# Kernel tuning notes

Measured on AMD Instinct MI355X. Metric: run time of the kernel, lower is better.

## Reference

```python
import math
import jax, jax.numpy as jnp
from jax import lax
import numpy as np

D = 128            # head_dim
B = 16             # independent KV streams (e.g., heads)
S = 4096           # update sequence length
P = 4096           # reconstruction positions
MAX_SEQ_LEN = 8192
# (n_waves, ema_rate, freq_low, freq_high) per level, coarse -> fine
LEVELS = [(16, 0.001, 0.01, 1.0), (32, 0.005, 0.5, 3.0), (64, 0.02, 1.0, 6.0), (128, 0.05, 2.0, 10.0), (256, 0.1, 4.0, 20.0)]
TWO_PI = 2.0 * math.pi


def setup_inputs() -> dict:
    key = jax.random.key(0)
    ks = jax.random.split(key, 2 + len(LEVELS))
    inp = {}
    inp['kv_vectors'] = jax.random.normal(ks[0], (B, S, D), dtype=jnp.float32)
    inp['positions'] = jnp.arange(S, dtype=jnp.int32)
    inp['recon_positions'] = jnp.sort(jax.random.randint(ks[1], (P,), 0, MAX_SEQ_LEN, dtype=jnp.int32))
    for i, (n, a, lo, hi) in enumerate(LEVELS):
        k1, k2 = jax.random.split(ks[2 + i], 2)
        inp[f'W_enc_{i}'] = jax.random.normal(k1, (3 * n, D), dtype=jnp.float32) / math.sqrt(D)
        inp[f'W_dec_{i}'] = jax.random.normal(k2, (D, n), dtype=jnp.float32) / math.sqrt(n)
        inp[f'base_freqs_{i}'] = jnp.linspace(lo, hi, n, dtype=jnp.float32)
    return inp


def _ema_final(x, alpha):
    # x: [S, ...]; returns EMA state after S sequential steps from zero init.
    def step(c, xt):
        return (1.0 - alpha) * c + alpha * xt, None
    final, _ = lax.scan(step, jnp.zeros(x.shape[1:], x.dtype), x)
    return final


def _forward(kv_vectors, positions, recon_positions, params):
    pos_norm = positions.astype(jnp.float32)[:, None] / MAX_SEQ_LEN    # [S,1]
    rpos_norm = recon_positions.astype(jnp.float32)[:, None] / MAX_SEQ_LEN  # [P,1]
    out = jnp.zeros((kv_vectors.shape[0], recon_positions.shape[0], D), jnp.float32)
    for (n, alpha, _lo, _hi), (W_enc, W_dec, base_freqs) in zip(LEVELS, params):
        deltas = jnp.einsum('bsd,wd->bsw', kv_vectors, W_enc)          # [B,S,3n]
        d_freq, d_amp, d_phase = jnp.split(deltas, 3, axis=-1)         # each [B,S,n]
        pos_signal = jnp.sin(base_freqs[None, :] * pos_norm * TWO_PI)  # [S,n]
        xs = jnp.stack([d_freq * pos_signal[None], jnp.abs(d_amp), d_phase], axis=0)  # [3,B,S,n]
        xs = jnp.transpose(xs, (2, 0, 1, 3))                           # [S,3,B,n]
        freqs, amps, phases = _ema_final(xs, alpha)                    # each [B,n]
        wave_phases = TWO_PI * (freqs[:, None, :] + base_freqs[None, None, :]) * rpos_norm[None] + phases[:, None, :]
        wave_values = amps[:, None, :] * jnp.sin(wave_phases)          # [B,P,n]
        out = out + jnp.einsum('bpn,dn->bpd', wave_values, W_dec)
    return out


def reference(kv_vectors, positions, recon_positions,
              W_enc_0, W_dec_0, base_freqs_0,
              W_enc_1, W_dec_1, base_freqs_1,
              W_enc_2, W_dec_2, base_freqs_2,
              W_enc_3, W_dec_3, base_freqs_3,
              W_enc_4, W_dec_4, base_freqs_4):
    params = [(W_enc_0, W_dec_0, base_freqs_0), (W_enc_1, W_dec_1, base_freqs_1),
              (W_enc_2, W_dec_2, base_freqs_2), (W_enc_3, W_dec_3, base_freqs_3),
              (W_enc_4, W_dec_4, base_freqs_4)]
    return _forward(kv_vectors, positions, recon_positions, params)
```

## Files before the change

### kernel.cpp

```cpp
#include <hip/hip_runtime.h>

typedef __attribute__((ext_vector_type(8))) short short8;
typedef __attribute__((ext_vector_type(4))) float floatx4;

#define B_   16
#define S_   4096
#define D_   128
#define P_   4096
#define CTOT 496
#define BP   (B_ * CTOT)
#define WPADG 512
#define INV2PI 0.15915494309189535f
#define NWAVE_B 132
#define NJB 33

__device__ __forceinline__ unsigned short f2bf(float f) {
    unsigned u = __float_as_uint(f);
    u += 0x7fffu + ((u >> 16) & 1u);
    return (unsigned short)(u >> 16);
}
__device__ __forceinline__ unsigned int pack2(float a, float b) {
    return (unsigned int)f2bf(a) | ((unsigned int)f2bf(b) << 16);
}

__global__ __launch_bounds__(256) void encoder(
    const float* __restrict__ kv, const int* __restrict__ positions,
    const float* __restrict__ we0, const float* __restrict__ we1,
    const float* __restrict__ we2, const float* __restrict__ we3,
    const float* __restrict__ we4,
    const float* __restrict__ wd0, const float* __restrict__ wd1,
    const float* __restrict__ wd2, const float* __restrict__ wd3,
    const float* __restrict__ wd4,
    const float* __restrict__ bf0, const float* __restrict__ bf1,
    const float* __restrict__ bf2, const float* __restrict__ bf3,
    const float* __restrict__ bf4,
    float* __restrict__ accb,
    unsigned short* __restrict__ wdbT)
{
    const int tid = threadIdx.x;

    if (blockIdx.y == 0) {
        int g = blockIdx.x * 256 + tid;
        int k0 = g * 8;
        if (k0 < D_ * WPADG) {
            int d = k0 >> 9, w0g = k0 & 511;
            union { unsigned int u[4]; short8 s; } r;
            if (w0g >= CTOT) {
                r.u[0] = r.u[1] = r.u[2] = r.u[3] = 0;
            } else {
                const float* src; int off, nl;
                if (w0g < 16)       { src = wd0; off = 0;   nl = 16;  }
                else if (w0g < 48)  { src = wd1; off = 16;  nl = 32;  }
                else if (w0g < 112) { src = wd2; off = 48;  nl = 64;  }
                else if (w0g < 240) { src = wd3; off = 112; nl = 128; }
                else                { src = wd4; off = 240; nl = 256; }
                const float* p = src + (size_t)d * nl + (w0g - off);
                float4 a = *(const float4*)(p);
                float4 c = *(const float4*)(p + 4);
                r.u[0] = pack2(a.x, a.y); r.u[1] = pack2(a.z, a.w);
                r.u[2] = pack2(c.x, c.y); r.u[3] = pack2(c.z, c.w);
            }
            *(short8*)(wdbT + k0) = r.s;
        }
    }

    const int b    = blockIdx.y;
    const int rem  = blockIdx.x * 4 + (tid >> 6);
    const int lane = tid & 63, ln15 = lane & 15, quad = lane >> 4;

    int bx, widx, nw;
    if (rem < 40)      { bx = rem / 10;               widx = rem % 10; nw = 10; }
    else if (rem < 60) { int r = rem - 40; bx = 4 + r / 5; widx = r % 5; nw = 5; }
    else if (rem < 84) { int r = rem - 60; bx = 8 + r / 3; widx = r % 3; nw = 3; }
    else               { bx = 16 + (rem - 84);        widx = 0;        nw = 1; }
    const int t0  = S_ - 64 * (bx + 1);
    const int cnt = (bx < 4) ? 93 : (bx < 8) ? 45 : (bx < 16) ? 21 : 9;

    const float* arow = kv + ((size_t)(b * S_ + t0 + ln15)) * D_ + quad * 8;
    short8 afr[4][4];
    #pragma unroll
    for (int m = 0; m < 4; ++m)
        #pragma unroll
        for (int k = 0; k < 4; ++k) {
            float4 x = *(const float4*)(arow + m * 16 * D_ + k * 32);
            float4 y = *(const float4*)(arow + m * 16 * D_ + k * 32 + 4);
            union { unsigned int u[4]; short8 s; } r;
            r.u[0] = pack2(x.x, x.y); r.u[1] = pack2(x.z, x.w);
            r.u[2] = pack2(y.x, y.y); r.u[3] = pack2(y.z, y.w);
            afr[m][k] = r.s;
        }

    const int   n_l[5]  = {16, 32, 64, 128, 256};
    const int   coff[5] = {0, 16, 48, 112, 240};
    const float al[5]   = {0.001f, 0.005f, 0.02f, 0.05f, 0.1f};
    const float l2m[5]  = {-0.0014434169f, -0.0072315692f, -0.0291463449f,
                           -0.0740005794f, -0.1520030934f};

    int   lprev = -1;
    float wtr[16];

    for (int ch = widx; ch < cnt; ch += nw) {
        int c = ch, l = 0;
        if (c >= 3) { c -= 3; l = 1;
            if (c >= 6) { c -= 6; l = 2;
                if (c >= 12) { c -= 12; l = 3;
                    if (c >= 24) { c -= 24; l = 4; } } } }
        const int ci = c, n = n_l[l];

        if (l != lprev) {
            lprev = l;
            const float s1 = (float)(S_ - 1 - t0);
            #pragma unroll
            for (int i = 0; i < 16; ++i) {
                float trel = (float)((i >> 2) * 16 + quad * 4 + (i & 3));
                wtr[i] = al[l] * exp2f((s1 - trel) * l2m[l]);
            }
        }

        const float* wel = (l == 0) ? we0 : (l == 1) ? we1 :
                           (l == 2) ? we2 : (l == 3) ? we3 : we4;
        const float* wrow = wel + (size_t)(ci * 16 + ln15) * D_ + quad * 8;

        floatx4 acc[4];
        #pragma unroll
        for (int m = 0; m < 4; ++m) acc[m] = (floatx4){0.f, 0.f, 0.f, 0.f};
        #pragma unroll
        for (int k = 0; k < 4; ++k) {
            float4 x = *(const float4*)(wrow + k * 32);
            float4 y = *(const float4*)(wrow + k * 32 + 4);
            union { unsigned int u[4]; short8 s; } r;
            r.u[0] = pack2(x.x, x.y); r.u[1] = pack2(x.z, x.w);
            r.u[2] = pack2(y.x, y.y); r.u[3] = pack2(y.z, y.w);
            #pragma unroll
            for (int m = 0; m < 4; ++m)
                acc[m] = __builtin_amdgcn_mfma_f32_16x16x32_bf16(
                             afr[m][k], r.s, acc[m], 0, 0, 0);
        }

        const int kind  = (ci * 16) / n;
        const int local = ci * 16 + ln15 - kind * n;
        float s = 0.0f;
        if (kind == 0) {
            const float* bfl = (l == 0) ? bf0 : (l == 1) ? bf1 :
                               (l == 2) ? bf2 : (l == 3) ? bf3 : bf4;
            const float bsv = bfl[local];
            #pragma unroll
            for (int m = 0; m < 4; ++m) {
                int4 pi = *(const int4*)(positions + t0 + m * 16 + quad * 4);
                float pfv[4] = {(float)pi.x, (float)pi.y, (float)pi.z, (float)pi.w};
                #pragma unroll
                for (int r = 0; r < 4; ++r) {
                    float rev = bsv * pfv[r] * (1.0f / 8192.0f);
                    rev -= floorf(rev);
                    s += wtr[m * 4 + r] * acc[m][r] * __builtin_amdgcn_sinf(rev);
                }
            }
        } else if (kind == 1) {
            #pragma unroll
            for (int m = 0; m < 4; ++m)
                #pragma unroll
                for (int r = 0; r < 4; ++r)
                    s += wtr[m * 4 + r] * fabsf(acc[m][r]);
        } else {
            #pragma unroll
            for (int m = 0; m < 4; ++m)
                #pragma unroll
                for (int r = 0; r < 4; ++r)
                    s += wtr[m * 4 + r] * acc[m][r];
        }
        s += __shfl_xor(s, 16);
        s += __shfl_xor(s, 32);
        if (lane < 16)
            atomicAdd(accb + (size_t)kind * BP + b * CTOT + coff[l] + local, s);
    }
}

__global__ __launch_bounds__(256) void decoder(
    const float* __restrict__ accb,
    const float* __restrict__ b0, const float* __restrict__ b1,
    const float* __restrict__ b2, const float* __restrict__ b3,
    const float* __restrict__ b4,
    const unsigned short* __restrict__ wdbT, const int* __restrict__ rpos,
    float* __restrict__ out)
{
    __shared__ unsigned short v[64 * 264];
    __shared__ float rpn[64];
    const int b = blockIdx.y, p0 = blockIdx.x * 64, tid = threadIdx.x;
    if (tid < 64) rpn[tid] = (float)rpos[p0 + tid] * (1.0f / 8192.0f);

    float Qv[2], Av[2], Pv[2];
    #pragma unroll
    for (int h = 0; h < 2; ++h) {
        int w = h * 256 + tid;
        float A = 0.f, Q = 0.f, P = 0.f;
        if (w < CTOT) {
            const float* bfl; int off;
            if (w < 16)       { bfl = b0; off = 0;   }
            else if (w < 48)  { bfl = b1; off = 16;  }
            else if (w < 112) { bfl = b2; off = 48;  }
            else if (w < 240) { bfl = b3; off = 112; }
            else              { bfl = b4; off = 240; }
            float f  = accb[0 * BP + b * CTOT + w];
            A        = accb[1 * BP + b * CTOT + w];
            float ph = accb[2 * BP + b * CTOT + w];
            Q = f + bfl[w - off];
            P = ph * INV2PI;
        }
        Qv[h] = Q; Av[h] = A; Pv[h] = P;
    }

    const int wid = tid >> 6, lane = tid & 63, ln = lane & 15, quad = lane >> 4;
    const int nt0 = wid * 2;

    floatx4 acc[4][2];
    #pragma unroll
    for (int m = 0; m < 4; ++m)
        #pragma unroll
        for (int j = 0; j < 2; ++j) acc[m][j] = (floatx4){0.f, 0.f, 0.f, 0.f};

    #pragma unroll
    for (int half = 0; half < 2; ++half) {
        const int w0 = half * 256;
        const float Q = Qv[half], A = Av[half], Ph = Pv[half];
        __syncthreads();
        for (int p = 0; p < 64; ++p) {
            float r = fmaf(Q, rpn[p], Ph);
            r -= floorf(r);
            v[p * 264 + tid] = f2bf(A * __builtin_amdgcn_sinf(r));
        }
        __syncthreads();

        #pragma unroll
        for (int kk = 0; kk < 8; ++kk) {
            short8 bn[2];
            #pragma unroll
            for (int j = 0; j < 2; ++j)
                bn[j] = *(const short8*)(wdbT + (size_t)((nt0 + j) * 16 + ln) * WPADG
                                         + w0 + kk * 32 + quad * 8);
            short8 am[4];
            #pragma unroll
            for (int m = 0; m < 4; ++m)
                am[m] = *(const short8*)&v[(m * 16 + ln) * 264 + kk * 32 + quad * 8];
            #pragma unroll
            for (int m = 0; m < 4; ++m)
                #pragma unroll
                for (int j = 0; j < 2; ++j)
                    acc[m][j] = __builtin_amdgcn_mfma_f32_16x16x32_bf16(
                                    am[m], bn[j], acc[m][j], 0, 0, 0);
        }
    }

    #pragma unroll
    for (int m = 0; m < 4; ++m)
        #pragma unroll
        for (int j = 0; j < 2; ++j)
            #pragma unroll
            for (int r = 0; r < 4; ++r) {
                int p = p0 + m * 16 + quad * 4 + r;
                int d = (nt0 + j) * 16 + ln;
                out[((size_t)(b * P_ + p)) * D_ + d] = acc[m][j][r];
            }
}

extern "C" void kernel_launch(void* const* d_in, const int* in_sizes, int n_in,
                              void* d_out, int out_size, void* d_ws, size_t ws_size,
                              hipStream_t stream)
{
    const float* kv        = (const float*)d_in[0];
    const int*   positions = (const int*)d_in[1];
    const int*   rpos      = (const int*)d_in[2];

    char* ws = (char*)d_ws;
    float*          accb = (float*)(ws + 0);
    unsigned short* wdbT = (unsigned short*)(ws + 95232);

    hipMemsetAsync(accb, 0, (size_t)(3 * BP) * sizeof(float), stream);

    encoder<<<dim3(NJB, B_), 256, 0, stream>>>(
        kv, positions,
        (const float*)d_in[3], (const float*)d_in[6], (const float*)d_in[9],
        (const float*)d_in[12], (const float*)d_in[15],
        (const float*)d_in[4], (const float*)d_in[7], (const float*)d_in[10],
        (const float*)d_in[13], (const float*)d_in[16],
        (const float*)d_in[5], (const float*)d_in[8], (const float*)d_in[11],
        (const float*)d_in[14], (const float*)d_in[17],
        accb, wdbT);

    decoder<<<dim3(P_ / 64, B_), 256, 0, stream>>>(
        accb,
        (const float*)d_in[5], (const float*)d_in[8], (const float*)d_in[11],
        (const float*)d_in[14], (const float*)d_in[17],
        wdbT, rpos, (float*)d_out);
}
```

Measured before the change: 180.2 us.

## Stage KV tile in shared memory and give each wave one encoder chunk

```diff
diff --git a/kernel.cpp b/kernel.cpp
--- a/kernel.cpp
+++ b/kernel.cpp
@@ -11,8 +11,7 @@
 #define BP   (B_ * CTOT)
 #define WPADG 512
 #define INV2PI 0.15915494309189535f
-#define NWAVE_B 132
-#define NJB 33
+#define NJB 336
 
 __device__ __forceinline__ unsigned short f2bf(float f) {
     unsigned u = __float_as_uint(f);
@@ -37,142 +36,135 @@
     float* __restrict__ accb,
     unsigned short* __restrict__ wdbT)
 {
+    __shared__ unsigned short kvb[64 * 136];
+    __shared__ float pf[64];
     const int tid = threadIdx.x;
-
-    if (blockIdx.y == 0) {
-        int g = blockIdx.x * 256 + tid;
-        int k0 = g * 8;
-        if (k0 < D_ * WPADG) {
-            int d = k0 >> 9, w0g = k0 & 511;
-            union { unsigned int u[4]; short8 s; } r;
-            if (w0g >= CTOT) {
-                r.u[0] = r.u[1] = r.u[2] = r.u[3] = 0;
-            } else {
-                const float* src; int off, nl;
-                if (w0g < 16)       { src = wd0; off = 0;   nl = 16;  }
-                else if (w0g < 48)  { src = wd1; off = 16;  nl = 32;  }
-                else if (w0g < 112) { src = wd2; off = 48;  nl = 64;  }
-                else if (w0g < 240) { src = wd3; off = 112; nl = 128; }
-                else                { src = wd4; off = 240; nl = 256; }
-                const float* p = src + (size_t)d * nl + (w0g - off);
-                float4 a = *(const float4*)(p);
-                float4 c = *(const float4*)(p + 4);
-                r.u[0] = pack2(a.x, a.y); r.u[1] = pack2(a.z, a.w);
-                r.u[2] = pack2(c.x, c.y); r.u[3] = pack2(c.z, c.w);
-            }
-            *(short8*)(wdbT + k0) = r.s;
-        }
-    }
-
-    const int b    = blockIdx.y;
-    const int rem  = blockIdx.x * 4 + (tid >> 6);
-    const int lane = tid & 63, ln15 = lane & 15, quad = lane >> 4;
-
-    int bx, widx, nw;
-    if (rem < 40)      { bx = rem / 10;               widx = rem % 10; nw = 10; }
-    else if (rem < 60) { int r = rem - 40; bx = 4 + r / 5; widx = r % 5; nw = 5; }
-    else if (rem < 84) { int r = rem - 60; bx = 8 + r / 3; widx = r % 3; nw = 3; }
-    else               { bx = 16 + (rem - 84);        widx = 0;        nw = 1; }
+    const int b   = blockIdx.y;
+    const int bid = blockIdx.x;
+
+    if (b == 0 && bid < 32) {
+        int k0 = (bid * 256 + tid) * 8;
+        int d = k0 >> 9, w0g = k0 & 511;
+        union { unsigned int u[4]; short8 s; } r;
+        if (w0g >= CTOT) {
+            r.u[0] = r.u[1] = r.u[2] = r.u[3] = 0;
+        } else {
+            const float* src; int off, nl;
+            if (w0g < 16)       { src = wd0; off = 0;   nl = 16;  }
+            else if (w0g < 48)  { src = wd1; off = 16;  nl = 32;  }
+            else if (w0g < 112) { src = wd2; off = 48;  nl = 64;  }
+            else if (w0g < 240) { src = wd3; off = 112; nl = 128; }
+            else                { src = wd4; off = 240; nl = 256; }
+            const float* p = src + (size_t)d * nl + (w0g - off);
+            float4 a = *(const float4*)(p);
+            float4 c = *(const float4*)(p + 4);
+            r.u[0] = pack2(a.x, a.y); r.u[1] = pack2(a.z, a.w);
+            r.u[2] = pack2(c.x, c.y); r.u[3] = pack2(c.z, c.w);
+        }
+        *(short8*)(wdbT + k0) = r.s;
+    }
+
+    int bx, lb;
+    if (bid < 96)       { bx = bid / 24;            lb = bid % 24; }
+    else if (bid < 144) { int r = bid - 96;  bx = 4 + r / 12; lb = r % 12; }
+    else if (bid < 192) { int r = bid - 144; bx = 8 + r / 6;  lb = r % 6;  }
+    else                { int r = bid - 192; bx = 16 + r / 3; lb = r % 3;  }
     const int t0  = S_ - 64 * (bx + 1);
     const int cnt = (bx < 4) ? 93 : (bx < 8) ? 45 : (bx < 16) ? 21 : 9;
 
-    const float* arow = kv + ((size_t)(b * S_ + t0 + ln15)) * D_ + quad * 8;
-    short8 afr[4][4];
-    #pragma unroll
-    for (int m = 0; m < 4; ++m)
-        #pragma unroll
-        for (int k = 0; k < 4; ++k) {
-            float4 x = *(const float4*)(arow + m * 16 * D_ + k * 32);
-            float4 y = *(const float4*)(arow + m * 16 * D_ + k * 32 + 4);
-            union { unsigned int u[4]; short8 s; } r;
-            r.u[0] = pack2(x.x, x.y); r.u[1] = pack2(x.z, x.w);
-            r.u[2] = pack2(y.x, y.y); r.u[3] = pack2(y.z, y.w);
-            afr[m][k] = r.s;
-        }
-
+    const float* src = kv + ((size_t)(b * S_ + t0)) * D_;
+    #pragma unroll
+    for (int f = 0; f < 8; ++f) {
+        int idx = f * 256 + tid;
+        int t = idx >> 5, d4 = idx & 31;
+        float4 val = *(const float4*)(src + t * D_ + d4 * 4);
+        unsigned long long u = (unsigned long long)pack2(val.x, val.y)
+                             | ((unsigned long long)pack2(val.z, val.w) << 32);
+        *(unsigned long long*)&kvb[t * 136 + d4 * 4] = u;
+    }
+    if (tid < 64) pf[tid] = (float)positions[t0 + tid] * (1.0f / 8192.0f);
+    __syncthreads();
+
+    const int wid = tid >> 6, lane = tid & 63, ln15 = lane & 15, quad = lane >> 4;
+    const int jid = lb * 4 + wid;
+    if (jid >= cnt) return;
+
+    int c = jid, l = 0;
+    if (c >= 3) { c -= 3; l = 1;
+        if (c >= 6) { c -= 6; l = 2;
+            if (c >= 12) { c -= 12; l = 3;
+                if (c >= 24) { c -= 24; l = 4; } } } }
+    const int ci = c;
     const int   n_l[5]  = {16, 32, 64, 128, 256};
     const int   coff[5] = {0, 16, 48, 112, 240};
     const float al[5]   = {0.001f, 0.005f, 0.02f, 0.05f, 0.1f};
     const float l2m[5]  = {-0.0014434169f, -0.0072315692f, -0.0291463449f,
                            -0.0740005794f, -0.1520030934f};
-
-    int   lprev = -1;
+    const int n = n_l[l];
+
     float wtr[16];
-
-    for (int ch = widx; ch < cnt; ch += nw) {
-        int c = ch, l = 0;
-        if (c >= 3) { c -= 3; l = 1;
-            if (c >= 6) { c -= 6; l = 2;
-                if (c >= 12) { c -= 12; l = 3;
-                    if (c >= 24) { c -= 24; l = 4; } } } }
-        const int ci = c, n = n_l[l];
-
-        if (l != lprev) {
-            lprev = l;
-            const float s1 = (float)(S_ - 1 - t0);
-            #pragma unroll
-            for (int i = 0; i < 16; ++i) {
-                float trel = (float)((i >> 2) * 16 + quad * 4 + (i & 3));
-                wtr[i] = al[l] * exp2f((s1 - trel) * l2m[l]);
+    {
+        const float s1 = (float)(S_ - 1 - t0);
+        #pragma unroll
+        for (int i = 0; i < 16; ++i) {
+            float trel = (float)((i >> 2) * 16 + quad * 4 + (i & 3));
+            wtr[i] = al[l] * exp2f((s1 - trel) * l2m[l]);
+        }
+    }
+
+    const float* wel = (l == 0) ? we0 : (l == 1) ? we1 :
+                       (l == 2) ? we2 : (l == 3) ? we3 : we4;
+    const float* wrow = wel + (size_t)(ci * 16 + ln15) * D_ + quad * 8;
+
+    floatx4 acc[4];
+    #pragma unroll
+    for (int m = 0; m < 4; ++m) acc[m] = (floatx4){0.f, 0.f, 0.f, 0.f};
+    #pragma unroll
+    for (int k = 0; k < 4; ++k) {
+        float4 x = *(const float4*)(wrow + k * 32);
+        float4 y = *(const float4*)(wrow + k * 32 + 4);
+        union { unsigned int u[4]; short8 s; } r;
+        r.u[0] = pack2(x.x, x.y); r.u[1] = pack2(x.z, x.w);
+        r.u[2] = pack2(y.x, y.y); r.u[3] = pack2(y.z, y.w);
+        #pragma unroll
+        for (int m = 0; m < 4; ++m) {
+            short8 af = *(const short8*)&kvb[(m * 16 + ln15) * 136 + k * 32 + quad * 8];
+            acc[m] = __builtin_amdgcn_mfma_f32_16x16x32_bf16(af, r.s, acc[m], 0, 0, 0);
+        }
+    }
+
+    const int kind  = (ci * 16) / n;
+    const int local = ci * 16 + ln15 - kind * n;
+    float s = 0.0f;
+    if (kind == 0) {
+        const float* bfl = (l == 0) ? bf0 : (l == 1) ? bf1 :
+                           (l == 2) ? bf2 : (l == 3) ? bf3 : bf4;
+        const float bsv = bfl[local];
+        #pragma unroll
+        for (int m = 0; m < 4; ++m)
+            #pragma unroll
+            for (int r = 0; r < 4; ++r) {
+                float rev = bsv * pf[m * 16 + quad * 4 + r];
+                rev -= floorf(rev);
+                s += wtr[m * 4 + r] * acc[m][r] * __builtin_amdgcn_sinf(rev);
             }
-        }
-
-        const float* wel = (l == 0) ? we0 : (l == 1) ? we1 :
-                           (l == 2) ? we2 : (l == 3) ? we3 : we4;
-        const float* wrow = wel + (size_t)(ci * 16 + ln15) * D_ + quad * 8;
-
-        floatx4 acc[4];
-        #pragma unroll
-        for (int m = 0; m < 4; ++m) acc[m] = (floatx4){0.f, 0.f, 0.f, 0.f};
-        #pragma unroll
-        for (int k = 0; k < 4; ++k) {
-            float4 x = *(const float4*)(wrow + k * 32);
-            float4 y = *(const float4*)(wrow + k * 32 + 4);
-            union { unsigned int u[4]; short8 s; } r;
-            r.u[0] = pack2(x.x, x.y); r.u[1] = pack2(x.z, x.w);
-            r.u[2] = pack2(y.x, y.y); r.u[3] = pack2(y.z, y.w);
-            #pragma unroll
-            for (int m = 0; m < 4; ++m)
-                acc[m] = __builtin_amdgcn_mfma_f32_16x16x32_bf16(
-                             afr[m][k], r.s, acc[m], 0, 0, 0);
-        }
-
-        const int kind  = (ci * 16) / n;
-        const int local = ci * 16 + ln15 - kind * n;
-        float s = 0.0f;
-        if (kind == 0) {
-            const float* bfl = (l == 0) ? bf0 : (l == 1) ? bf1 :
-                               (l == 2) ? bf2 : (l == 3) ? bf3 : bf4;
-            const float bsv = bfl[local];
-            #pragma unroll
-            for (int m = 0; m < 4; ++m) {
-                int4 pi = *(const int4*)(positions + t0 + m * 16 + quad * 4);
-                float pfv[4] = {(float)pi.x, (float)pi.y, (float)pi.z, (float)pi.w};
-                #pragma unroll
-                for (int r = 0; r < 4; ++r) {
-                    float rev = bsv * pfv[r] * (1.0f / 8192.0f);
-                    rev -= floorf(rev);
-                    s += wtr[m * 4 + r] * acc[m][r] * __builtin_amdgcn_sinf(rev);
-                }
-            }
-        } else if (kind == 1) {
-            #pragma unroll
-            for (int m = 0; m < 4; ++m)
-                #pragma unroll
-                for (int r = 0; r < 4; ++r)
-                    s += wtr[m * 4 + r] * fabsf(acc[m][r]);
-        } else {
-            #pragma unroll
-            for (int m = 0; m < 4; ++m)
-                #pragma unroll
-                for (int r = 0; r < 4; ++r)
-                    s += wtr[m * 4 + r] * acc[m][r];
-        }
-        s += __shfl_xor(s, 16);
-        s += __shfl_xor(s, 32);
-        if (lane < 16)
-            atomicAdd(accb + (size_t)kind * BP + b * CTOT + coff[l] + local, s);
-    }
+    } else if (kind == 1) {
+        #pragma unroll
+        for (int m = 0; m < 4; ++m)
+            #pragma unroll
+            for (int r = 0; r < 4; ++r)
+                s += wtr[m * 4 + r] * fabsf(acc[m][r]);
+    } else {
+        #pragma unroll
+        for (int m = 0; m < 4; ++m)
+            #pragma unroll
+            for (int r = 0; r < 4; ++r)
+                s += wtr[m * 4 + r] * acc[m][r];
+    }
+    s += __shfl_xor(s, 16);
+    s += __shfl_xor(s, 32);
+    if (lane < 16)
+        atomicAdd(accb + (size_t)kind * BP + b * CTOT + coff[l] + local, s);
 }
 
 __global__ __launch_bounds__(256) void decoder(
```

Result: faster. 166.0 us (-7.9%).
